# Kernel optimization log

Hardware: AMD Instinct MI355X
Metric: run time of the kernel (lower is better)

Reference implementation:

```python
import jax, jax.numpy as jnp
import numpy as np

D_MODEL = 512
N_HEADS = 8
D_HEAD = D_MODEL // N_HEADS
LN_EPS = 1e-5
SCALE = 1.0 / (D_HEAD ** 0.5)


def _rel_shift(x):
    # Faithful port of the TF _rel_shift: x is (b, i, j, n)
    x = jnp.transpose(x, (2, 0, 1, 3))          # (j, b, i, n)
    j, b, i, n = x.shape
    x = jnp.pad(x, ((0, 0), (1, 0), (0, 0), (0, 0)))  # (j, b+1, i, n)
    x = x.reshape(b + 1, j, i, n)
    x = x[1:]                                    # (b, j, i, n)
    x = x.reshape(j, b, i, n)
    x = jnp.transpose(x, (1, 0, 2, 3))           # back to (b, i, j, n) layout
    return x


def setup_inputs() -> dict:
    key = jax.random.key(0)
    ks = jax.random.split(key, 12)
    B, S = 8, 1024
    std = 0.01
    inp = {
        "inputs": jax.random.normal(ks[0], (B, S, D_MODEL), jnp.float32),
        "pos_embed": jax.random.normal(ks[1], (B, S, D_MODEL), jnp.float32),
        "mask": jnp.ones((B, S, S), jnp.float32),
        "Wq": jax.random.normal(ks[2], (D_MODEL, D_MODEL), jnp.float32) * std,
        "bq": jnp.zeros((D_MODEL,), jnp.float32),
        "Wk": jax.random.normal(ks[3], (D_MODEL, D_MODEL), jnp.float32) * std,
        "bk": jnp.zeros((D_MODEL,), jnp.float32),
        "Wv": jax.random.normal(ks[4], (D_MODEL, D_MODEL), jnp.float32) * std,
        "bv": jnp.zeros((D_MODEL,), jnp.float32),
        "Wo": jax.random.normal(ks[5], (D_MODEL, D_MODEL), jnp.float32) * std,
        "u_bias": jax.random.normal(ks[6], (N_HEADS, D_HEAD), jnp.float32) * std,
        "v_bias": jax.random.normal(ks[7], (N_HEADS, D_HEAD), jnp.float32) * std,
        "gamma": 1.0 + 0.02 * jax.random.normal(ks[8], (D_MODEL,), jnp.float32),
        "beta": 0.02 * jax.random.normal(ks[9], (D_MODEL,), jnp.float32),
    }
    return inp


def reference(inputs, pos_embed, mask, Wq, bq, Wk, bk, Wv, bv, Wo, u_bias, v_bias, gamma, beta):
    B, S, _ = inputs.shape
    # LayerNorm (note: TF code reassigns `inputs` to the normalized value,
    # so the residual uses the NORMALIZED input)
    mu = jnp.mean(inputs, axis=-1, keepdims=True)
    var = jnp.mean(jnp.square(inputs - mu), axis=-1, keepdims=True)
    x = (inputs - mu) * jax.lax.rsqrt(var + LN_EPS) * gamma + beta

    q = (x @ Wq + bq).reshape(B, S, N_HEADS, D_HEAD)
    k = (x @ Wk + bk).reshape(B, S, N_HEADS, D_HEAD)
    v = (x @ Wv + bv).reshape(B, S, N_HEADS, D_HEAD)
    p = pos_embed.reshape(B, S, N_HEADS, D_HEAD)

    content_score = jnp.einsum("bind,bjnd->bijn", q + u_bias, k)
    pos_score = jnp.einsum("bind,bjnd->bijn", q + v_bias, p)
    pos_score = _rel_shift(pos_score)
    score = (content_score + pos_score) * SCALE

    score = jnp.where(mask[..., None] == 0.0, jnp.finfo(jnp.float32).min, score)
    attn = jax.nn.softmax(score, axis=2)  # softmax over key axis j (axis 2)

    ctx = jnp.einsum("bijn,bjnd->bind", attn, v).reshape(B, S, D_MODEL)
    out = ctx @ Wo  # no bias
    return out + x
```

## Files before the change

### kernel.cpp

```cpp
#include <hip/hip_runtime.h>
#include <hip/hip_bf16.h>


typedef __attribute__((ext_vector_type(8))) short short8;
typedef __attribute__((ext_vector_type(4))) float floatx4;

static __device__ __forceinline__ floatx4 mfma16(short8 a, short8 b, floatx4 c) {
  return __builtin_amdgcn_mfma_f32_16x16x32_bf16(a, b, c, 0, 0, 0);
}
static __device__ __forceinline__ float redsum16(float v) {
  v += __shfl_xor(v, 1);
  v += __shfl_xor(v, 2);
  v += __shfl_xor(v, 4);
  v += __shfl_xor(v, 8);
  return v;
}

#define SCL 0.1803368801111244f

__global__ __launch_bounds__(256) void prep_kernel(
    const float* __restrict__ Wq, const float* __restrict__ Wk,
    const float* __restrict__ Wv, const float* __restrict__ Wo,
    const float* __restrict__ pos, __hip_bfloat16* __restrict__ WT,
    __hip_bfloat16* __restrict__ P)
{
  __shared__ float t[64][65];
  const int bid = blockIdx.x, tid = threadIdx.x;
  if (bid < 256) {
    const int w = bid >> 6, i0 = ((bid >> 3) & 7) * 64, o0 = (bid & 7) * 64;
    const float* W = (w == 0) ? Wq : (w == 1) ? Wk : (w == 2) ? Wv : Wo;
    #pragma unroll
    for (int it = 0; it < 16; ++it) {
      int idx = tid + it * 256, r = idx >> 6, c = idx & 63;
      t[r][c] = W[(size_t)(i0 + r) * 512 + o0 + c];
    }
    __syncthreads();
    #pragma unroll
    for (int it = 0; it < 16; ++it) {
      int idx = tid + it * 256, r = idx >> 6, c = idx & 63;
      WT[(size_t)w * 262144 + (size_t)(o0 + r) * 512 + i0 + c] = __float2bfloat16(t[c][r]);
    }
  } else {
    size_t id = (size_t)(bid - 256) * 256 + tid;
    float4 v = ((const float4*)pos)[id];
    __hip_bfloat16 h[4] = {__float2bfloat16(v.x), __float2bfloat16(v.y),
                           __float2bfloat16(v.z), __float2bfloat16(v.w)};
    ((ulong1*)P)[id] = *(ulong1*)h;
  }
}

__global__ __launch_bounds__(256) void ln_kernel(
    const float* __restrict__ inp, const float* __restrict__ gamma,
    const float* __restrict__ beta, float* __restrict__ xf,
    __hip_bfloat16* __restrict__ xb)
{
  const int row = blockIdx.x;
  const int t = threadIdx.x;
  const float* rp = inp + (size_t)row * 512;
  float2 v = *(const float2*)(rp + t * 2);
  float s = v.x + v.y;
  float sq = v.x * v.x + v.y * v.y;
  #pragma unroll
  for (int m = 1; m < 64; m <<= 1) { s += __shfl_xor(s, m); sq += __shfl_xor(sq, m); }
  __shared__ float ssum[4], ssqs[4];
  int w = t >> 6;
  if ((t & 63) == 0) { ssum[w] = s; ssqs[w] = sq; }
  __syncthreads();
  s  = ssum[0] + ssum[1] + ssum[2] + ssum[3];
  sq = ssqs[0] + ssqs[1] + ssqs[2] + ssqs[3];
  float mu  = s * (1.0f / 512.0f);
  float var = sq * (1.0f / 512.0f) - mu * mu;
  float rstd = 1.0f / sqrtf(var + 1e-5f);
  float2 g  = *(const float2*)(gamma + t * 2);
  float2 be = *(const float2*)(beta + t * 2);
  float o0 = (v.x - mu) * rstd * g.x + be.x;
  float o1 = (v.y - mu) * rstd * g.y + be.y;
  *(float2*)(xf + (size_t)row * 512 + t * 2) = make_float2(o0, o1);
  __hip_bfloat16 h2[2] = {__float2bfloat16(o0), __float2bfloat16(o1)};
  *(unsigned int*)(xb + (size_t)row * 512 + t * 2) = *(unsigned int*)h2;
}

__global__ __launch_bounds__(256) void gemm_qkv(
    const __hip_bfloat16* __restrict__ X, const __hip_bfloat16* __restrict__ WT,
    const float* __restrict__ bq, const float* __restrict__ bk,
    const float* __restrict__ bv, const float* __restrict__ ub,
    const float* __restrict__ vbias,
    __hip_bfloat16* __restrict__ QU, __hip_bfloat16* __restrict__ QV,
    __hip_bfloat16* __restrict__ Kb, __hip_bfloat16* __restrict__ VT)
{
  __shared__ __hip_bfloat16 SM[2 * 128 * 72];
  __hip_bfloat16* As = SM;
  __hip_bfloat16* Bs = SM + 128 * 72;
  const int tid = threadIdx.x;
  const int m0 = blockIdx.x * 128;
  const int nb = blockIdx.y;
  const int n0 = nb * 128;
  const int wave = tid >> 6, lane = tid & 63, lg = lane >> 4, li = lane & 15;
  const int wm = wave >> 1, wn = wave & 1;
  const floatx4 ZERO4 = {0.f, 0.f, 0.f, 0.f};
  floatx4 acc[4][4];
  #pragma unroll
  for (int i = 0; i < 4; ++i)
    #pragma unroll
    for (int j = 0; j < 4; ++j) acc[i][j] = ZERO4;

  for (int k0 = 0; k0 < 512; k0 += 64) {
    __syncthreads();
    #pragma unroll
    for (int it = 0; it < 4; ++it) {
      int idx = tid + it * 256, r = idx >> 3, c = (idx & 7) * 8;
      *(uint4*)&As[r * 72 + c] = *(const uint4*)(X  + (size_t)(m0 + r) * 512 + k0 + c);
      *(uint4*)&Bs[r * 72 + c] = *(const uint4*)(WT + (size_t)(n0 + r) * 512 + k0 + c);
    }
    __syncthreads();
    #pragma unroll
    for (int kk = 0; kk < 2; ++kk) {
      short8 a[4], b[4];
      #pragma unroll
      for (int ms = 0; ms < 4; ++ms)
        a[ms] = *(const short8*)&As[(wm * 64 + ms * 16 + li) * 72 + kk * 32 + lg * 8];
      #pragma unroll
      for (int ns = 0; ns < 4; ++ns)
        b[ns] = *(const short8*)&Bs[(wn * 64 + ns * 16 + li) * 72 + kk * 32 + lg * 8];
      #pragma unroll
      for (int ms = 0; ms < 4; ++ms)
        #pragma unroll
        for (int ns = 0; ns < 4; ++ns)
          acc[ms][ns] = mfma16(a[ms], b[ns], acc[ms][ns]);
    }
  }

  if (nb < 8) {
    #pragma unroll
    for (int ms = 0; ms < 4; ++ms)
      #pragma unroll
      for (int ns = 0; ns < 4; ++ns) {
        int nl = wn * 64 + ns * 16 + li;
        int n = n0 + nl;
        #pragma unroll
        for (int rr = 0; rr < 4; ++rr) {
          size_t m = m0 + wm * 64 + ms * 16 + lg * 4 + rr;
          float val = acc[ms][ns][rr];
          if (nb < 4) {
            float vq = val + bq[n];
            QU[m * 512 + n] = __float2bfloat16((vq + ub[n]) * SCL);
            QV[m * 512 + n] = __float2bfloat16((vq + vbias[n]) * SCL);
          } else {
            int nk = n - 512;
            Kb[m * 512 + nk] = __float2bfloat16(val + bk[nk]);
          }
        }
      }
  } else {
    __hip_bfloat16* Tt = SM;
    __syncthreads();
    #pragma unroll
    for (int ms = 0; ms < 4; ++ms)
      #pragma unroll
      for (int ns = 0; ns < 4; ++ns) {
        int nl = wn * 64 + ns * 16 + li;
        int nv = n0 - 1024 + nl;
        float bvv = bv[nv];
        #pragma unroll
        for (int rr = 0; rr < 4; ++rr) {
          int ml = wm * 64 + ms * 16 + lg * 4 + rr;
          Tt[nl * 136 + ml] = __float2bfloat16(acc[ms][ns][rr] + bvv);
        }
      }
    __syncthreads();
    const int b = blockIdx.x >> 3, s0 = (blockIdx.x & 7) * 128;
    #pragma unroll
    for (int it = 0; it < 8; ++it) {
      int idx = tid + it * 256;
      int drow = idx >> 4, c16 = idx & 15;
      uint4 val = *(const uint4*)&Tt[drow * 136 + c16 * 8];
      int dg = n0 - 1024 + drow;
      int head = dg >> 6, d = dg & 63;
      *(uint4*)(VT + (size_t)((b * 8 + head) * 64 + d) * 1024 + s0 + c16 * 8) = val;
    }
  }
}

__global__ __launch_bounds__(128) void attn_fused(
    const __hip_bfloat16* __restrict__ QU, const __hip_bfloat16* __restrict__ QV,
    const __hip_bfloat16* __restrict__ Kb, const __hip_bfloat16* __restrict__ VT,
    const __hip_bfloat16* __restrict__ P,  __hip_bfloat16* __restrict__ ctx)
{
  __shared__ __hip_bfloat16 Ks[64 * 64];
  __shared__ __hip_bfloat16 Qs[64 * 64];
  __shared__ __hip_bfloat16 Vs[64 * 64];
  __shared__ __hip_bfloat16 Pw[2][32 * 64];

  const int wid = ((int)blockIdx.x & 7) * 144 + ((int)blockIdx.x >> 3);
  const int b = wid / 144;
  const int rem = wid - b * 144;
  const int n = rem / 18;
  const int rem2 = rem - n * 18;
  const int r = rem2 >> 1, hf = rem2 & 1;
  const int bp = (b + 7 - r) % 9;
  const int sb = bp - 1;
  const int Nr = (r < 7) ? 114 : 113;

  const int tid = threadIdx.x;
  const int w = tid >> 6, lane = tid & 63;
  const int lg = lane >> 4, li = lane & 15;
  const short8 ZS = {0, 0, 0, 0, 0, 0, 0, 0};
  const floatx4 ZERO4 = {0.f, 0.f, 0.f, 0.f};

  short8 qf[2][2], pg[2][2];
  #pragma unroll
  for (int at = 0; at < 2; ++at) {
    int t = hf * 64 + w * 32 + at * 16 + li;
    if (t > Nr - 1) t = Nr - 1;
    int alpha = r + 9 * t;
    const __hip_bfloat16* qp = QU + ((size_t)(b * 1024 + alpha)) * 512 + n * 64;
    qf[at][0] = *(const short8*)(qp + lg * 8);
    qf[at][1] = *(const short8*)(qp + 32 + lg * 8);
    pg[at][0] = ZS; pg[at][1] = ZS;
    if (bp > 0) {
      int js = (8 * alpha + b + 1024 - bp) / 9;
      const __hip_bfloat16* pp = P + ((size_t)(sb * 1024 + js)) * 512 + n * 64;
      pg[at][0] = *(const short8*)(pp + lg * 8);
      pg[at][1] = *(const short8*)(pp + 32 + lg * 8);
    }
  }

  floatx4 O[2][4];
  float lsum[2][4];
  #pragma unroll
  for (int at = 0; at < 2; ++at)
    #pragma unroll
    for (int j = 0; j < 4; ++j) { O[at][j] = ZERO4; lsum[at][j] = 0.f; }

  const __hip_bfloat16* Ksrc = Kb + ((size_t)(b * 1024)) * 512 + n * 64;
  const __hip_bfloat16* Qsrc = QV + ((size_t)((bp > 0 ? sb : 0) * 1024)) * 512 + n * 64;
  const __hip_bfloat16* Vsrc = VT + ((size_t)(b * 8 + n)) * 64 * 1024;
  __hip_bfloat16* pw = Pw[w];

  for (int c0 = 0; c0 < 1024; c0 += 64) {
    __syncthreads();
    #pragma unroll
    for (int it = 0; it < 4; ++it) {
      int idx = tid + it * 128, row = idx >> 3, sl = idx & 7;
      int dsl = (sl ^ (row & 7)) << 3;
      *(uint4*)&Ks[row * 64 + dsl] = *(const uint4*)(Ksrc + (size_t)(c0 + row) * 512 + sl * 8);
      *(uint4*)&Vs[row * 64 + dsl] = *(const uint4*)(Vsrc + (size_t)row * 1024 + c0 + sl * 8);
      if (bp > 0)
        *(uint4*)&Qs[row * 64 + dsl] = *(const uint4*)(Qsrc + (size_t)(c0 + row) * 512 + sl * 8);
    }
    __syncthreads();

    floatx4 s[2][4];
    #pragma unroll
    for (int at = 0; at < 2; ++at)
      #pragma unroll
      for (int bt = 0; bt < 4; ++bt) s[at][bt] = ZERO4;
    __builtin_amdgcn_s_setprio(1);
    #pragma unroll
    for (int bt = 0; bt < 4; ++bt) {
      int row = bt * 16 + li;
      #pragma unroll
      for (int h = 0; h < 2; ++h) {
        int off = row * 64 + ((h * 32 + lg * 8) ^ ((row & 7) << 3));
        short8 kf = *(const short8*)&Ks[off];
        s[0][bt] = mfma16(qf[0][h], kf, s[0][bt]);
        s[1][bt] = mfma16(qf[1][h], kf, s[1][bt]);
        if (bp > 0) {
          short8 qvf = *(const short8*)&Qs[off];
          s[0][bt] = mfma16(pg[0][h], qvf, s[0][bt]);
          s[1][bt] = mfma16(pg[1][h], qvf, s[1][bt]);
        }
      }
    }
    __builtin_amdgcn_s_setprio(0);

    #pragma unroll
    for (int at = 0; at < 2; ++at)
      #pragma unroll
      for (int bt = 0; bt < 4; ++bt)
        #pragma unroll
        for (int rr = 0; rr < 4; ++rr) {
          float pv = exp2f(s[at][bt][rr]);
          lsum[at][rr] += pv;
          int m = at * 16 + lg * 4 + rr;
          pw[m * 64 + ((bt * 16 + li) ^ ((m & 7) << 3))] = __float2bfloat16(pv);
        }

    short8 pa[2][2];
    #pragma unroll
    for (int at = 0; at < 2; ++at) {
      int rowp = at * 16 + li;
      pa[at][0] = *(const short8*)&pw[rowp * 64 + ((lg * 8) ^ ((rowp & 7) << 3))];
      pa[at][1] = *(const short8*)&pw[rowp * 64 + ((32 + lg * 8) ^ ((rowp & 7) << 3))];
    }
    __builtin_amdgcn_s_setprio(1);
    #pragma unroll
    for (int dt = 0; dt < 4; ++dt) {
      int rowv = dt * 16 + li;
      short8 v0 = *(const short8*)&Vs[rowv * 64 + ((lg * 8) ^ ((rowv & 7) << 3))];
      short8 v1 = *(const short8*)&Vs[rowv * 64 + ((32 + lg * 8) ^ ((rowv & 7) << 3))];
      O[0][dt] = mfma16(pa[0][0], v0, O[0][dt]);
      O[0][dt] = mfma16(pa[0][1], v1, O[0][dt]);
      O[1][dt] = mfma16(pa[1][0], v0, O[1][dt]);
      O[1][dt] = mfma16(pa[1][1], v1, O[1][dt]);
    }
    __builtin_amdgcn_s_setprio(0);
  }

  #pragma unroll
  for (int at = 0; at < 2; ++at)
    #pragma unroll
    for (int rr = 0; rr < 4; ++rr) {
      float lr = redsum16(lsum[at][rr]);
      int t = hf * 64 + w * 32 + at * 16 + lg * 4 + rr;
      if (t < Nr) {
        int alpha = r + 9 * t;
        float inv = 1.0f / lr;
        __hip_bfloat16* cp = ctx + ((size_t)(b * 1024 + alpha)) * 512 + n * 64;
        #pragma unroll
        for (int dt = 0; dt < 4; ++dt)
          cp[dt * 16 + li] = __float2bfloat16(O[at][dt][rr] * inv);
      }
    }
}

__global__ __launch_bounds__(256) void gemm_out(
    const __hip_bfloat16* __restrict__ A, const __hip_bfloat16* __restrict__ WoT,
    const float* __restrict__ xres, float* __restrict__ out)
{
  __shared__ __hip_bfloat16 As[128 * 72];
  __shared__ __hip_bfloat16 Bs[64 * 72];
  const int tid = threadIdx.x;
  const int m0 = blockIdx.x * 128, n0 = blockIdx.y * 64;
  const int wave = tid >> 6, lane = tid & 63, lg = lane >> 4, li = lane & 15;
  const int wm = wave >> 1, wn = wave & 1;
  const floatx4 ZERO4 = {0.f, 0.f, 0.f, 0.f};
  floatx4 acc[4][2];
  #pragma unroll
  for (int i = 0; i < 4; ++i)
    #pragma unroll
    for (int j = 0; j < 2; ++j) acc[i][j] = ZERO4;

  for (int k0 = 0; k0 < 512; k0 += 64) {
    __syncthreads();
    #pragma unroll
    for (int it = 0; it < 4; ++it) {
      int idx = tid + it * 256, rr = idx >> 3, c = (idx & 7) * 8;
      *(uint4*)&As[rr * 72 + c] = *(const uint4*)(A + (size_t)(m0 + rr) * 512 + k0 + c);
    }
    #pragma unroll
    for (int it = 0; it < 2; ++it) {
      int idx = tid + it * 256, rr = idx >> 3, c = (idx & 7) * 8;
      *(uint4*)&Bs[rr * 72 + c] = *(const uint4*)(WoT + (size_t)(n0 + rr) * 512 + k0 + c);
    }
    __syncthreads();
    #pragma unroll
    for (int kk = 0; kk < 2; ++kk) {
      short8 a[4], b[2];
      #pragma unroll
      for (int ms = 0; ms < 4; ++ms)
        a[ms] = *(const short8*)&As[(wm * 64 + ms * 16 + li) * 72 + kk * 32 + lg * 8];
      #pragma unroll
      for (int ns = 0; ns < 2; ++ns)
        b[ns] = *(const short8*)&Bs[(wn * 32 + ns * 16 + li) * 72 + kk * 32 + lg * 8];
      #pragma unroll
      for (int ms = 0; ms < 4; ++ms)
        #pragma unroll
        for (int ns = 0; ns < 2; ++ns)
          acc[ms][ns] = mfma16(a[ms], b[ns], acc[ms][ns]);
    }
  }
  #pragma unroll
  for (int ms = 0; ms < 4; ++ms)
    #pragma unroll
    for (int ns = 0; ns < 2; ++ns)
      #pragma unroll
      for (int rr = 0; rr < 4; ++rr) {
        size_t m = m0 + wm * 64 + ms * 16 + lg * 4 + rr;
        int nn = n0 + wn * 32 + ns * 16 + li;
        out[m * 512 + nn] = acc[ms][ns][rr] + xres[m * 512 + nn];
      }
}

extern "C" void kernel_launch(void* const* d_in, const int* in_sizes, int n_in,
                              void* d_out, int out_size, void* d_ws, size_t ws_size,
                              hipStream_t stream) {
  (void)in_sizes; (void)n_in; (void)out_size; (void)ws_size;
  const float* inputs = (const float*)d_in[0];
  const float* pos    = (const float*)d_in[1];
  const float* Wq = (const float*)d_in[3];
  const float* bq = (const float*)d_in[4];
  const float* Wk = (const float*)d_in[5];
  const float* bk = (const float*)d_in[6];
  const float* Wv = (const float*)d_in[7];
  const float* bv = (const float*)d_in[8];
  const float* Wo = (const float*)d_in[9];
  const float* ub = (const float*)d_in[10];
  const float* vb = (const float*)d_in[11];
  const float* gamma = (const float*)d_in[12];
  const float* beta  = (const float*)d_in[13];
  float* out = (float*)d_out;

  char* w = (char*)d_ws;
  const size_t MB = 1024 * 1024;
  float*          x_f32 = (float*)(w);
  __hip_bfloat16* x_bf  = (__hip_bfloat16*)(w + 16 * MB);
  __hip_bfloat16* P     = (__hip_bfloat16*)(w + 24 * MB);
  __hip_bfloat16* WT    = (__hip_bfloat16*)(w + 32 * MB);
  __hip_bfloat16* QU    = (__hip_bfloat16*)(w + 34 * MB);
  __hip_bfloat16* QV    = (__hip_bfloat16*)(w + 42 * MB);
  __hip_bfloat16* Kb    = (__hip_bfloat16*)(w + 50 * MB);
  __hip_bfloat16* VT    = (__hip_bfloat16*)(w + 58 * MB);
  __hip_bfloat16* ctx   = (__hip_bfloat16*)(w + 66 * MB);

  prep_kernel<<<4352, 256, 0, stream>>>(Wq, Wk, Wv, Wo, pos, WT, P);
  ln_kernel<<<8192, 256, 0, stream>>>(inputs, gamma, beta, x_f32, x_bf);
  gemm_qkv<<<dim3(64, 12), 256, 0, stream>>>(x_bf, WT, bq, bk, bv, ub, vb,
                                             QU, QV, Kb, VT);
  attn_fused<<<1152, 128, 0, stream>>>(QU, QV, Kb, VT, P, ctx);
  gemm_out<<<dim3(64, 8), 256, 0, stream>>>(ctx, WT + 3 * 262144, x_f32, out);
}
```

Measured before the change: 270.3 us.

## Double-buffer attention tiles via direct global-to-LDS loads with 8-wave blocks, merge prep+LN

The attention kernel now uses 512-thread blocks. Each block covers a full residue class with 8 waves of 16 query rows, where before two 128-thread blocks each took half. K, QV and V tiles are double-buffered in LDS and filled by global_load_lds, so the next chunk's loads overlap the current chunk's MFMA work. This replaces register-staged loads and the sync at the top of each iteration. The weight-prep and LayerNorm kernels are merged into one launch to save a launch. Risks: each wave now has fewer rows, so K/V data read from LDS is reused less per wave, and bp==0 blocks still load the unused QV tile. The vmcnt wait and barrier ordering must also be exactly right.

```diff
diff --git a/kernel.cpp b/kernel.cpp
--- a/kernel.cpp
+++ b/kernel.cpp
@@ -15,69 +15,73 @@
   v += __shfl_xor(v, 8);
   return v;
 }
+static __device__ __forceinline__ void gll16(const __hip_bfloat16* g, __hip_bfloat16* l) {
+  __builtin_amdgcn_global_load_lds(
+      (const __attribute__((address_space(1))) void*)g,
+      (__attribute__((address_space(3))) void*)l, 16, 0, 0);
+}
 
 #define SCL 0.1803368801111244f
-
-__global__ __launch_bounds__(256) void prep_kernel(
+#define LDP 72
+
+__global__ __launch_bounds__(256) void prep_ln_kernel(
+    const float* __restrict__ inp, const float* __restrict__ gamma,
+    const float* __restrict__ beta, float* __restrict__ xf,
+    __hip_bfloat16* __restrict__ xb,
     const float* __restrict__ Wq, const float* __restrict__ Wk,
     const float* __restrict__ Wv, const float* __restrict__ Wo,
     const float* __restrict__ pos, __hip_bfloat16* __restrict__ WT,
     __hip_bfloat16* __restrict__ P)
 {
-  __shared__ float t[64][65];
-  const int bid = blockIdx.x, tid = threadIdx.x;
-  if (bid < 256) {
-    const int w = bid >> 6, i0 = ((bid >> 3) & 7) * 64, o0 = (bid & 7) * 64;
+  __shared__ float smem[64][65];
+  const int bid = blockIdx.x, t = threadIdx.x;
+  if (bid < 8192) {
+    const int row = bid;
+    const float* rp = inp + (size_t)row * 512;
+    float2 v = *(const float2*)(rp + t * 2);
+    float s = v.x + v.y;
+    float sq = v.x * v.x + v.y * v.y;
+    #pragma unroll
+    for (int m = 1; m < 64; m <<= 1) { s += __shfl_xor(s, m); sq += __shfl_xor(sq, m); }
+    float* ssum = &smem[0][0];
+    float* ssqs = &smem[1][0];
+    int w = t >> 6;
+    if ((t & 63) == 0) { ssum[w] = s; ssqs[w] = sq; }
+    __syncthreads();
+    s  = ssum[0] + ssum[1] + ssum[2] + ssum[3];
+    sq = ssqs[0] + ssqs[1] + ssqs[2] + ssqs[3];
+    float mu  = s * (1.0f / 512.0f);
+    float var = sq * (1.0f / 512.0f) - mu * mu;
+    float rstd = 1.0f / sqrtf(var + 1e-5f);
+    float2 g  = *(const float2*)(gamma + t * 2);
+    float2 be = *(const float2*)(beta + t * 2);
+    float o0 = (v.x - mu) * rstd * g.x + be.x;
+    float o1 = (v.y - mu) * rstd * g.y + be.y;
+    *(float2*)(xf + (size_t)row * 512 + t * 2) = make_float2(o0, o1);
+    __hip_bfloat16 h2[2] = {__float2bfloat16(o0), __float2bfloat16(o1)};
+    *(unsigned int*)(xb + (size_t)row * 512 + t * 2) = *(unsigned int*)h2;
+  } else if (bid < 8448) {
+    const int wb = bid - 8192;
+    const int w = wb >> 6, i0 = ((wb >> 3) & 7) * 64, o0 = (wb & 7) * 64;
     const float* W = (w == 0) ? Wq : (w == 1) ? Wk : (w == 2) ? Wv : Wo;
     #pragma unroll
     for (int it = 0; it < 16; ++it) {
-      int idx = tid + it * 256, r = idx >> 6, c = idx & 63;
-      t[r][c] = W[(size_t)(i0 + r) * 512 + o0 + c];
+      int idx = t + it * 256, r = idx >> 6, c = idx & 63;
+      smem[r][c] = W[(size_t)(i0 + r) * 512 + o0 + c];
     }
     __syncthreads();
     #pragma unroll
     for (int it = 0; it < 16; ++it) {
-      int idx = tid + it * 256, r = idx >> 6, c = idx & 63;
-      WT[(size_t)w * 262144 + (size_t)(o0 + r) * 512 + i0 + c] = __float2bfloat16(t[c][r]);
+      int idx = t + it * 256, r = idx >> 6, c = idx & 63;
+      WT[(size_t)w * 262144 + (size_t)(o0 + r) * 512 + i0 + c] = __float2bfloat16(smem[c][r]);
     }
   } else {
-    size_t id = (size_t)(bid - 256) * 256 + tid;
+    size_t id = (size_t)(bid - 8448) * 256 + t;
     float4 v = ((const float4*)pos)[id];
     __hip_bfloat16 h[4] = {__float2bfloat16(v.x), __float2bfloat16(v.y),
                            __float2bfloat16(v.z), __float2bfloat16(v.w)};
     ((ulong1*)P)[id] = *(ulong1*)h;
   }
-}
-
-__global__ __launch_bounds__(256) void ln_kernel(
-    const float* __restrict__ inp, const float* __restrict__ gamma,
-    const float* __restrict__ beta, float* __restrict__ xf,
-    __hip_bfloat16* __restrict__ xb)
-{
-  const int row = blockIdx.x;
-  const int t = threadIdx.x;
-  const float* rp = inp + (size_t)row * 512;
-  float2 v = *(const float2*)(rp + t * 2);
-  float s = v.x + v.y;
-  float sq = v.x * v.x + v.y * v.y;
-  #pragma unroll
-  for (int m = 1; m < 64; m <<= 1) { s += __shfl_xor(s, m); sq += __shfl_xor(sq, m); }
-  __shared__ float ssum[4], ssqs[4];
-  int w = t >> 6;
-  if ((t & 63) == 0) { ssum[w] = s; ssqs[w] = sq; }
-  __syncthreads();
-  s  = ssum[0] + ssum[1] + ssum[2] + ssum[3];
-  sq = ssqs[0] + ssqs[1] + ssqs[2] + ssqs[3];
-  float mu  = s * (1.0f / 512.0f);
-  float var = sq * (1.0f / 512.0f) - mu * mu;
-  float rstd = 1.0f / sqrtf(var + 1e-5f);
-  float2 g  = *(const float2*)(gamma + t * 2);
-  float2 be = *(const float2*)(beta + t * 2);
-  float o0 = (v.x - mu) * rstd * g.x + be.x;
-  float o1 = (v.y - mu) * rstd * g.y + be.y;
-  *(float2*)(xf + (size_t)row * 512 + t * 2) = make_float2(o0, o1);
-  __hip_bfloat16 h2[2] = {__float2bfloat16(o0), __float2bfloat16(o1)};
-  *(unsigned int*)(xb + (size_t)row * 512 + t * 2) = *(unsigned int*)h2;
 }
 
 __global__ __launch_bounds__(256) void gemm_qkv(
@@ -181,22 +185,18 @@
   }
 }
 
-__global__ __launch_bounds__(128) void attn_fused(
+__global__ __launch_bounds__(512) void attn_fused(
     const __hip_bfloat16* __restrict__ QU, const __hip_bfloat16* __restrict__ QV,
     const __hip_bfloat16* __restrict__ Kb, const __hip_bfloat16* __restrict__ VT,
     const __hip_bfloat16* __restrict__ P,  __hip_bfloat16* __restrict__ ctx)
 {
-  __shared__ __hip_bfloat16 Ks[64 * 64];
-  __shared__ __hip_bfloat16 Qs[64 * 64];
-  __shared__ __hip_bfloat16 Vs[64 * 64];
-  __shared__ __hip_bfloat16 Pw[2][32 * 64];
-
-  const int wid = ((int)blockIdx.x & 7) * 144 + ((int)blockIdx.x >> 3);
-  const int b = wid / 144;
-  const int rem = wid - b * 144;
-  const int n = rem / 18;
-  const int rem2 = rem - n * 18;
-  const int r = rem2 >> 1, hf = rem2 & 1;
+  __shared__ __hip_bfloat16 Stage[2][3 * 64 * 64];
+  __shared__ __hip_bfloat16 Pw[8][16 * 64];
+
+  const int wid = ((int)blockIdx.x & 7) * 72 + ((int)blockIdx.x >> 3);
+  const int r = wid % 9;
+  const int n = (wid / 9) & 7;
+  const int b = wid / 72;
   const int bp = (b + 7 - r) % 9;
   const int sb = bp - 1;
   const int Nr = (r < 7) ? 114 : 113;
@@ -207,54 +207,70 @@
   const short8 ZS = {0, 0, 0, 0, 0, 0, 0, 0};
   const floatx4 ZERO4 = {0.f, 0.f, 0.f, 0.f};
 
-  short8 qf[2][2], pg[2][2];
-  #pragma unroll
-  for (int at = 0; at < 2; ++at) {
-    int t = hf * 64 + w * 32 + at * 16 + li;
+  short8 qf[2], pg[2];
+  {
+    int t = w * 16 + li;
     if (t > Nr - 1) t = Nr - 1;
     int alpha = r + 9 * t;
     const __hip_bfloat16* qp = QU + ((size_t)(b * 1024 + alpha)) * 512 + n * 64;
-    qf[at][0] = *(const short8*)(qp + lg * 8);
-    qf[at][1] = *(const short8*)(qp + 32 + lg * 8);
-    pg[at][0] = ZS; pg[at][1] = ZS;
+    qf[0] = *(const short8*)(qp + lg * 8);
+    qf[1] = *(const short8*)(qp + 32 + lg * 8);
+    pg[0] = ZS; pg[1] = ZS;
     if (bp > 0) {
       int js = (8 * alpha + b + 1024 - bp) / 9;
       const __hip_bfloat16* pp = P + ((size_t)(sb * 1024 + js)) * 512 + n * 64;
-      pg[at][0] = *(const short8*)(pp + lg * 8);
-      pg[at][1] = *(const short8*)(pp + 32 + lg * 8);
-    }
-  }
-
-  floatx4 O[2][4];
-  float lsum[2][4];
-  #pragma unroll
-  for (int at = 0; at < 2; ++at)
-    #pragma unroll
-    for (int j = 0; j < 4; ++j) { O[at][j] = ZERO4; lsum[at][j] = 0.f; }
-
-  const __hip_bfloat16* Ksrc = Kb + ((size_t)(b * 1024)) * 512 + n * 64;
+      pg[0] = *(const short8*)(pp + lg * 8);
+      pg[1] = *(const short8*)(pp + 32 + lg * 8);
+    }
+  }
+
+  const __hip_bfloat16* Ksrc = Kb + ((size_t)b * 1024) * 512 + n * 64;
   const __hip_bfloat16* Qsrc = QV + ((size_t)((bp > 0 ? sb : 0) * 1024)) * 512 + n * 64;
   const __hip_bfloat16* Vsrc = VT + ((size_t)(b * 8 + n)) * 64 * 1024;
-  __hip_bfloat16* pw = Pw[w];
-
-  for (int c0 = 0; c0 < 1024; c0 += 64) {
-    __syncthreads();
-    #pragma unroll
-    for (int it = 0; it < 4; ++it) {
-      int idx = tid + it * 128, row = idx >> 3, sl = idx & 7;
-      int dsl = (sl ^ (row & 7)) << 3;
-      *(uint4*)&Ks[row * 64 + dsl] = *(const uint4*)(Ksrc + (size_t)(c0 + row) * 512 + sl * 8);
-      *(uint4*)&Vs[row * 64 + dsl] = *(const uint4*)(Vsrc + (size_t)row * 1024 + c0 + sl * 8);
-      if (bp > 0)
-        *(uint4*)&Qs[row * 64 + dsl] = *(const uint4*)(Qsrc + (size_t)(c0 + row) * 512 + sl * 8);
-    }
-    __syncthreads();
-
-    floatx4 s[2][4];
-    #pragma unroll
-    for (int at = 0; at < 2; ++at)
-      #pragma unroll
-      for (int bt = 0; bt < 4; ++bt) s[at][bt] = ZERO4;
+
+  const __hip_bfloat16* gsrc[3];
+  int gbase[3], gmul[3], ldsoff[3];
+  {
+    int ls = lane >> 3, sl = lane & 7;
+    #pragma unroll
+    for (int j = 0; j < 3; ++j) {
+      int g = w * 3 + j;
+      int a = g >> 3, rg = g & 7;
+      int row = rg * 8 + ls;
+      int slx = (sl ^ (row & 7)) * 8;
+      gsrc[j] = (a == 0) ? Ksrc : (a == 1) ? Qsrc : Vsrc;
+      gbase[j] = (a < 2) ? (row * 512 + slx) : (row * 1024 + slx);
+      gmul[j] = (a < 2) ? 512 : 1;
+      ldsoff[j] = g * 512;
+    }
+  }
+
+  floatx4 O[4];
+  float lsum[4];
+  #pragma unroll
+  for (int j = 0; j < 4; ++j) { O[j] = ZERO4; lsum[j] = 0.f; }
+
+  #pragma unroll
+  for (int j = 0; j < 3; ++j)
+    gll16(gsrc[j] + gbase[j], &Stage[0][0] + ldsoff[j]);
+
+  int cur = 0;
+  for (int c = 0; c < 16; ++c) {
+    int nc0 = ((c + 1) & 15) * 64;
+    #pragma unroll
+    for (int j = 0; j < 3; ++j)
+      gll16(gsrc[j] + gbase[j] + nc0 * gmul[j], &Stage[cur ^ 1][0] + ldsoff[j]);
+    asm volatile("s_waitcnt vmcnt(3)" ::: "memory");
+    __builtin_amdgcn_s_barrier();
+    asm volatile("" ::: "memory");
+
+    const __hip_bfloat16* Ks = &Stage[cur][0];
+    const __hip_bfloat16* Qs = &Stage[cur][4096];
+    const __hip_bfloat16* Vs = &Stage[cur][8192];
+
+    floatx4 s[4];
+    #pragma unroll
+    for (int bt = 0; bt < 4; ++bt) s[bt] = ZERO4;
     __builtin_amdgcn_s_setprio(1);
     #pragma unroll
     for (int bt = 0; bt < 4; ++bt) {
@@ -263,65 +279,56 @@
       for (int h = 0; h < 2; ++h) {
         int off = row * 64 + ((h * 32 + lg * 8) ^ ((row & 7) << 3));
         short8 kf = *(const short8*)&Ks[off];
-        s[0][bt] = mfma16(qf[0][h], kf, s[0][bt]);
-        s[1][bt] = mfma16(qf[1][h], kf, s[1][bt]);
+        s[bt] = mfma16(qf[h], kf, s[bt]);
         if (bp > 0) {
           short8 qvf = *(const short8*)&Qs[off];
-          s[0][bt] = mfma16(pg[0][h], qvf, s[0][bt]);
-          s[1][bt] = mfma16(pg[1][h], qvf, s[1][bt]);
+          s[bt] = mfma16(pg[h], qvf, s[bt]);
         }
       }
     }
     __builtin_amdgcn_s_setprio(0);
 
     #pragma unroll
-    for (int at = 0; at < 2; ++at)
-      #pragma unroll
-      for (int bt = 0; bt < 4; ++bt)
-        #pragma unroll
-        for (int rr = 0; rr < 4; ++rr) {
-          float pv = exp2f(s[at][bt][rr]);
-          lsum[at][rr] += pv;
-          int m = at * 16 + lg * 4 + rr;
-          pw[m * 64 + ((bt * 16 + li) ^ ((m & 7) << 3))] = __float2bfloat16(pv);
-        }
-
-    short8 pa[2][2];
-    #pragma unroll
-    for (int at = 0; at < 2; ++at) {
-      int rowp = at * 16 + li;
-      pa[at][0] = *(const short8*)&pw[rowp * 64 + ((lg * 8) ^ ((rowp & 7) << 3))];
-      pa[at][1] = *(const short8*)&pw[rowp * 64 + ((32 + lg * 8) ^ ((rowp & 7) << 3))];
-    }
+    for (int bt = 0; bt < 4; ++bt)
+      #pragma unroll
+      for (int rr = 0; rr < 4; ++rr) {
+        float pv = exp2f(s[bt][rr]);
+        lsum[rr] += pv;
+        int m = lg * 4 + rr;
+        Pw[w][m * 64 + ((bt * 16 + li) ^ ((m & 7) << 3))] = __float2bfloat16(pv);
+      }
+
+    short8 pa0 = *(const short8*)&Pw[w][li * 64 + ((lg * 8) ^ ((li & 7) << 3))];
+    short8 pa1 = *(const short8*)&Pw[w][li * 64 + ((32 + lg * 8) ^ ((li & 7) << 3))];
     __builtin_amdgcn_s_setprio(1);
     #pragma unroll
     for (int dt = 0; dt < 4; ++dt) {
       int rowv = dt * 16 + li;
       short8 v0 = *(const short8*)&Vs[rowv * 64 + ((lg * 8) ^ ((rowv & 7) << 3))];
       short8 v1 = *(const short8*)&Vs[rowv * 64 + ((32 + lg * 8) ^ ((rowv & 7) << 3))];
-      O[0][dt] = mfma16(pa[0][0], v0, O[0][dt]);
-      O[0][dt] = mfma16(pa[0][1], v1, O[0][dt]);
-      O[1][dt] = mfma16(pa[1][0], v0, O[1][dt]);
-      O[1][dt] = mfma16(pa[1][1], v1, O[1][dt]);
+      O[dt] = mfma16(pa0, v0, O[dt]);
+      O[dt] = mfma16(pa1, v1, O[dt]);
     }
     __builtin_amdgcn_s_setprio(0);
-  }
-
-  #pragma unroll
-  for (int at = 0; at < 2; ++at)
-    #pragma unroll
-    for (int rr = 0; rr < 4; ++rr) {
-      float lr = redsum16(lsum[at][rr]);
-      int t = hf * 64 + w * 32 + at * 16 + lg * 4 + rr;
-      if (t < Nr) {
-        int alpha = r + 9 * t;
-        float inv = 1.0f / lr;
-        __hip_bfloat16* cp = ctx + ((size_t)(b * 1024 + alpha)) * 512 + n * 64;
-        #pragma unroll
-        for (int dt = 0; dt < 4; ++dt)
-          cp[dt * 16 + li] = __float2bfloat16(O[at][dt][rr] * inv);
-      }
-    }
+
+    __builtin_amdgcn_s_barrier();
+    asm volatile("" ::: "memory");
+    cur ^= 1;
+  }
+
+  #pragma unroll
+  for (int rr = 0; rr < 4; ++rr) {
+    float lr = redsum16(lsum[rr]);
+    int t = w * 16 + lg * 4 + rr;
+    if (t < Nr) {
+      int alpha = r + 9 * t;
+      float inv = 1.0f / lr;
+      __hip_bfloat16* cp = ctx + ((size_t)(b * 1024 + alpha)) * 512 + n * 64;
+      #pragma unroll
+      for (int dt = 0; dt < 4; ++dt)
+        cp[dt * 16 + li] = __float2bfloat16(O[dt][rr] * inv);
+    }
+  }
 }
 
 __global__ __launch_bounds__(256) void gemm_out(
@@ -413,10 +420,10 @@
   __hip_bfloat16* VT    = (__hip_bfloat16*)(w + 58 * MB);
   __hip_bfloat16* ctx   = (__hip_bfloat16*)(w + 66 * MB);
 
-  prep_kernel<<<4352, 256, 0, stream>>>(Wq, Wk, Wv, Wo, pos, WT, P);
-  ln_kernel<<<8192, 256, 0, stream>>>(inputs, gamma, beta, x_f32, x_bf);
+  prep_ln_kernel<<<12544, 256, 0, stream>>>(inputs, gamma, beta, x_f32, x_bf,
+                                            Wq, Wk, Wv, Wo, pos, WT, P);
   gemm_qkv<<<dim3(64, 12), 256, 0, stream>>>(x_bf, WT, bq, bk, bv, ub, vb,
                                              QU, QV, Kb, VT);
-  attn_fused<<<1152, 128, 0, stream>>>(QU, QV, Kb, VT, P, ctx);
+  attn_fused<<<576, 512, 0, stream>>>(QU, QV, Kb, VT, P, ctx);
   gemm_out<<<dim3(64, 8), 256, 0, stream>>>(ctx, WT + 3 * 262144, x_f32, out);
 }
```

Result: faster. 238.0 us (-12.0%).
